# Performance work log

Measured on AMD Instinct MI355X. Metric: run time of the kernel, lower is better.

## Reference

```python
import jax, jax.numpy as jnp
import numpy as np

B, T_AUX, UP = 4, 75, 110
N_AUX, N_Q, HID, SKIP = 54, 256, 192, 256
K, AUX_K = 6, 3
DIL_FACTS = [0, 1, 2] * 3  # dilation_depth=3, dilation_repeat=3
T = T_AUX * UP - 1  # 8249


def conv1d(x, w, b, dil=1, pad=(0, 0)):
    # x: (B,C,T), w: (O,I,K) torch Conv1d layout
    if pad != (0, 0):
        x = jnp.pad(x, ((0, 0), (0, 0), pad))
    y = jax.lax.conv_general_dilated(x, w, (1,), 'VALID', rhs_dilation=(dil,),
                                     dimension_numbers=('NCH', 'OIH', 'NCH'))
    return y + b[None, :, None]


def setup_inputs() -> dict:
    key = jax.random.key(0)
    ks = jax.random.split(key, 24)
    s = 0.05
    inp = {
        'audio': jax.random.normal(ks[0], (B, N_Q, T), jnp.float32),
        'aux': jax.random.normal(ks[1], (B, N_AUX, T_AUX), jnp.float32),
        'scale_in_w': jax.random.normal(ks[2], (N_AUX, N_AUX, 1), jnp.float32) * s,
        'scale_in_b': jax.random.normal(ks[3], (N_AUX,), jnp.float32) * s,
        'aux0_w': jax.random.normal(ks[4], (N_AUX * 3, N_AUX, AUX_K), jnp.float32) * s,
        'aux0_b': jax.random.normal(ks[5], (N_AUX * 3,), jnp.float32) * s,
        'aux1_w': jax.random.normal(ks[6], (N_AUX * 9, N_AUX * 3, AUX_K), jnp.float32) * s,
        'aux1_b': jax.random.normal(ks[7], (N_AUX * 9,), jnp.float32) * s,
        'up_w': jax.random.normal(ks[8], (UP,), jnp.float32) * s,
        'up_b': jax.random.normal(ks[9], (), jnp.float32) * s,
        'causal_w': jax.random.normal(ks[10], (HID, N_Q, K), jnp.float32) * s,
        'causal_b': jax.random.normal(ks[11], (HID,), jnp.float32) * s,
        'inx_w': jax.random.normal(ks[12], (9, 2 * HID, N_AUX * 9, 1), jnp.float32) * s,
        'inx_b': jax.random.normal(ks[13], (9, 2 * HID), jnp.float32) * s,
        'dilh_w': jax.random.normal(ks[14], (9, 2 * HID, HID, K), jnp.float32) * s,
        'dilh_b': jax.random.normal(ks[15], (9, 2 * HID), jnp.float32) * s,
        'skip_w': jax.random.normal(ks[16], (9, SKIP, HID, 1), jnp.float32) * s,
        'skip_b': jax.random.normal(ks[17], (9, SKIP), jnp.float32) * s,
        'out1_w': jax.random.normal(ks[18], (N_Q, SKIP, 1), jnp.float32) * s,
        'out1_b': jax.random.normal(ks[19], (N_Q,), jnp.float32) * s,
        'out2_w': jax.random.normal(ks[20], (N_Q, N_Q, 1), jnp.float32) * s,
        'out2_b': jax.random.normal(ks[21], (N_Q,), jnp.float32) * s,
    }
    return inp


def reference(audio, aux, scale_in_w, scale_in_b, aux0_w, aux0_b, aux1_w, aux1_b,
              up_w, up_b, causal_w, causal_b, inx_w, inx_b, dilh_w, dilh_b,
              skip_w, skip_b, out1_w, out1_b, out2_w, out2_b):
    # conditioning path: scale_in -> two-sided dilated convs -> deconv upsample
    a = conv1d(aux, scale_in_w, scale_in_b)
    a = conv1d(a, aux0_w, aux0_b, dil=1, pad=(1, 1))      # k=3, dil=1, same length
    a = conv1d(a, aux1_w, aux1_b, dil=3, pad=(3, 3))      # k=3, dil=3, same length
    b_, c_, t_ = a.shape
    x = (a[:, :, :, None] * up_w).reshape(b_, c_, t_ * UP) + up_b  # ConvTranspose2d(1,1,(1,UP))
    x = x[:, :, 1:]  # (B, 486, T)
    # audio path: causal conv (left pad k-1) + softsign
    h = jax.nn.soft_sign(conv1d(audio, causal_w, causal_b, dil=1, pad=(K - 1, 0)))
    sum_out = None
    for l, d in enumerate(DIL_FACTS):
        dil = K ** d
        lpad = dil * (K - 1)  # k**(d+1) - k**d
        xh = conv1d(x, inx_w[l], inx_b[l]) * conv1d(h, dilh_w[l], dilh_b[l], dil=dil, pad=(lpad, 0))
        z = jax.nn.sigmoid(xh[:, :HID])
        h = (1.0 - z) * jnp.tanh(xh[:, HID:]) + z * h
        skip = conv1d(h, skip_w[l], skip_b[l])
        sum_out = skip if sum_out is None else sum_out + skip
    out = conv1d(jax.nn.relu(sum_out), out1_w, out1_b)
    out = conv1d(jax.nn.relu(out), out2_w, out2_b)
    return out.transpose(0, 2, 1)  # (B, T, n_quantize)
```

## Files before the change

### kernel.cpp

```cpp
#include <hip/hip_runtime.h>

#define TLEN 8249
#define TPAD 8256
#define NTILES 129
#define NB 4
#define NAUX 54
#define NQ 256
#define HID 192
#define NSKIP 256
#define KW 6
#define UPF 110
#define TAUX 75
#define PADR 180
#define HROWS (PADR + TPAD)

typedef __attribute__((ext_vector_type(8))) short bf16x8v;
typedef __attribute__((ext_vector_type(4))) float f32x4;

__device__ __forceinline__ unsigned short f2bf(float f) {
  unsigned int u = __float_as_uint(f);
  u += 0x7FFFu + ((u >> 16) & 1u);
  return (unsigned short)(u >> 16);
}

__device__ __forceinline__ f32x4 mfma16(bf16x8v a, bf16x8v b, f32x4 c) {
  return __builtin_amdgcn_mfma_f32_16x16x32_bf16(a, b, c, 0, 0, 0);
}

__global__ void prepack_kernel(
    const float* causal_w, const float* dilh_w, const float* skip_w,
    const float* out1_w, const float* out2_w,
    const float* inx_w, const float* inx_b, const float* up_b,
    unsigned short* pk_causal, unsigned short* pk_dilh, unsigned short* pk_skip,
    unsigned short* pk_out1, unsigned short* pk_out2, float* Cbuf)
{
  int i = blockIdx.x * blockDim.x + threadIdx.x;
  if (i < 9*6*6*24*64*8) {
    int t = i;
    int j = t & 7; t >>= 3;
    int lane = t & 63; t >>= 6;
    int nf = t % 24; t /= 24;
    int kc = t % 6; t /= 6;
    int tap = t % 6; t /= 6;
    int l = t;
    int oc = nf*16 + (lane & 15);
    int ic = kc*32 + ((lane >> 4) << 3) + j;
    pk_dilh[i] = f2bf(dilh_w[((l*384 + oc)*HID + ic)*KW + tap]);
  }
  if (i < 6*8*12*64*8) {
    int t = i;
    int j = t & 7; t >>= 3;
    int lane = t & 63; t >>= 6;
    int nf = t % 12; t /= 12;
    int kc = t % 8; t /= 8;
    int tap = t;
    int oc = nf*16 + (lane & 15);
    int ic = kc*32 + ((lane >> 4) << 3) + j;
    pk_causal[i] = f2bf(causal_w[(oc*NQ + ic)*KW + tap]);
  }
  if (i < 9*6*16*64*8) {
    int t = i;
    int j = t & 7; t >>= 3;
    int lane = t & 63; t >>= 6;
    int nf = t % 16; t /= 16;
    int kc = t % 6; t /= 6;
    int l = t;
    int sc = nf*16 + (lane & 15);
    int ic = kc*32 + ((lane >> 4) << 3) + j;
    pk_skip[i] = f2bf(skip_w[(l*NSKIP + sc)*HID + ic]);
  }
  if (i < 8*16*64*8) {
    int t = i;
    int j = t & 7; t >>= 3;
    int lane = t & 63; t >>= 6;
    int nf = t % 16; t /= 16;
    int kc = t;
    int oq = nf*16 + (lane & 15);
    int sc = kc*32 + ((lane >> 4) << 3) + j;
    pk_out1[i] = f2bf(out1_w[oq*NSKIP + sc]);
    pk_out2[i] = f2bf(out2_w[oq*NQ + sc]);
  }
  if (i < 9*384) {
    int l = i / 384, oc = i % 384;
    const float* wr = inx_w + (l*384 + oc)*486;
    float s = 0.f;
    for (int c = 0; c < 486; c++) s += wr[c];
    Cbuf[i] = up_b[0]*s + inx_b[i];
  }
}

__global__ void zpad_kernel(unsigned short* hA, unsigned short* hB) {
  int i = blockIdx.x*blockDim.x + threadIdx.x;
  if (i < NB*PADR*HID) {
    int b = i / (PADR*HID), r = i % (PADR*HID);
    hA[(size_t)(b*HROWS)*HID + r] = 0;
    hB[(size_t)(b*HROWS)*HID + r] = 0;
  }
}

__global__ void aux1_kernel(const float* aux, const float* w, const float* bias, float* a1) {
  int q = blockIdx.x, b = blockIdx.y, co = threadIdx.x;
  if (co >= NAUX) return;
  float acc = bias[co];
  for (int ci = 0; ci < NAUX; ci++)
    acc += w[co*NAUX + ci] * aux[(b*NAUX + ci)*TAUX + q];
  a1[(b*NAUX + co)*TAUX + q] = acc;
}

__global__ void aux2_kernel(const float* a1, const float* w, const float* bias, float* a2) {
  __shared__ float s[3][NAUX];
  int q = blockIdx.x, b = blockIdx.y, tid = threadIdx.x;
  for (int i = tid; i < 3*NAUX; i += blockDim.x) {
    int k = i / NAUX, c = i % NAUX;
    int qq = q - 1 + k;
    s[k][c] = (qq >= 0 && qq < TAUX) ? a1[(b*NAUX + c)*TAUX + qq] : 0.f;
  }
  __syncthreads();
  int co = tid;
  if (co >= 162) return;
  float acc = bias[co];
  for (int c = 0; c < NAUX; c++)
    #pragma unroll
    for (int k = 0; k < 3; k++)
      acc += w[(co*NAUX + c)*3 + k] * s[k][c];
  a2[(b*162 + co)*TAUX + q] = acc;
}

__global__ void aux3_kernel(const float* a2, const float* w, const float* bias, float* a3) {
  __shared__ float s[3][162];
  int q = blockIdx.x, b = blockIdx.y, tid = threadIdx.x;
  for (int i = tid; i < 3*162; i += blockDim.x) {
    int k = i / 162, c = i % 162;
    int qq = q + 3*(k - 1);
    s[k][c] = (qq >= 0 && qq < TAUX) ? a2[(b*162 + c)*TAUX + qq] : 0.f;
  }
  __syncthreads();
  int co = tid;
  if (co >= 486) return;
  float acc = bias[co];
  for (int c = 0; c < 162; c++)
    #pragma unroll
    for (int k = 0; k < 3; k++)
      acc += w[(co*162 + c)*3 + k] * s[k][c];
  a3[(b*486 + co)*TAUX + q] = acc;
}

__global__ void g_kernel(const float* a3, const float* inx_w, float* G) {
  __shared__ float s[486][15];
  int q0 = blockIdx.x * 15, b = blockIdx.y, l = blockIdx.z;
  int tid = threadIdx.x;
  for (int i = tid; i < 486*15; i += 384) {
    int c = i / 15, qq = i % 15;
    s[c][qq] = a3[(b*486 + c)*TAUX + q0 + qq];
  }
  __syncthreads();
  int oc = tid;
  float acc[15];
  #pragma unroll
  for (int qq = 0; qq < 15; qq++) acc[qq] = 0.f;
  const float* wrow = inx_w + (l*384 + oc)*486;
  for (int c = 0; c < 486; c++) {
    float w = wrow[c];
    #pragma unroll
    for (int qq = 0; qq < 15; qq++) acc[qq] += w * s[c][qq];
  }
  for (int qq = 0; qq < 15; qq++)
    G[((size_t)(l*NB + b)*TAUX + q0 + qq)*384 + oc] = acc[qq];
}

__global__ __launch_bounds__(256, 2)
void causal_kernel(const float* audio, const unsigned short* pk, const float* cb,
                   float* hf, unsigned short* hbf)
{
  __shared__ __align__(16) unsigned short sA[72*264];
  int b = blockIdx.y, t0 = blockIdx.x*64, tid = threadIdx.x;
  int wv = tid >> 6, lane = tid & 63, lanelo = lane & 15;

  for (int i = tid; i < 72*256; i += 256) {
    int ic = i / 72, tt = i % 72;
    int t = t0 - 5 + tt;
    float v = (t >= 0 && t < TLEN) ? audio[(size_t)(b*NQ + ic)*TLEN + t] : 0.f;
    sA[tt*264 + ic] = f2bf(v);
  }
  __syncthreads();

  f32x4 acc[4][3];
  f32x4 z4 = {0.f, 0.f, 0.f, 0.f};
  #pragma unroll
  for (int m = 0; m < 4; m++)
    #pragma unroll
    for (int i = 0; i < 3; i++) acc[m][i] = z4;

  for (int tap = 0; tap < 6; tap++) {
    for (int kc = 0; kc < 8; kc++) {
      bf16x8v A[4];
      int ko = kc*32 + ((lane >> 4) << 3);
      #pragma unroll
      for (int m = 0; m < 4; m++)
        A[m] = *(const bf16x8v*)&sA[(m*16 + lanelo + tap)*264 + ko];
      #pragma unroll
      for (int i = 0; i < 3; i++) {
        int nf = wv*3 + i;
        bf16x8v Bf = *(const bf16x8v*)&pk[(size_t)((((tap*8) + kc)*12 + nf)*64 + lane)*8];
        #pragma unroll
        for (int m = 0; m < 4; m++) acc[m][i] = mfma16(A[m], Bf, acc[m][i]);
      }
    }
  }

  #pragma unroll
  for (int m = 0; m < 4; m++)
    #pragma unroll
    for (int i = 0; i < 3; i++) {
      int oc = (wv*3 + i)*16 + lanelo;
      float bias = cb[oc];
      #pragma unroll
      for (int r = 0; r < 4; r++) {
        int tl = m*16 + ((lane >> 4) << 2) + r;
        int t = t0 + tl;
        float v = acc[m][i][r] + bias;
        float h0 = v / (1.f + fabsf(v));
        hf[(size_t)(b*TPAD + t)*HID + oc] = h0;
        hbf[(size_t)(b*HROWS + t + PADR)*HID + oc] = f2bf(h0);
      }
    }
}

__global__ __launch_bounds__(256, 2)
void layer_kernel(int dil, int first,
                  const unsigned short* hin, unsigned short* hout,
                  float* hf, float* sum_out,
                  const unsigned short* pk_dilh_l, const float* dilh_b_l,
                  const unsigned short* pk_skip_l, const float* skip_b_l,
                  const float* Gl, const float* Cl, const float* up_w)
{
  __shared__ __align__(16) unsigned short hs[64*200];
  int b = blockIdx.y, t0 = blockIdx.x*64, tid = threadIdx.x;
  int wv = tid >> 6, lane = tid & 63, lanelo = lane & 15;

  f32x4 accz[4][3], acct[4][3];
  f32x4 z4 = {0.f, 0.f, 0.f, 0.f};
  #pragma unroll
  for (int m = 0; m < 4; m++)
    #pragma unroll
    for (int i = 0; i < 3; i++) { accz[m][i] = z4; acct[m][i] = z4; }

  for (int tap = 0; tap < 6; tap++) {
    __syncthreads();
    int rowbase = t0 + (tap - 5)*dil + PADR;
    for (int i = tid; i < 64*24; i += 256) {
      int r = i / 24, seg = i % 24;
      bf16x8v v = *(const bf16x8v*)&hin[(size_t)(b*HROWS + rowbase + r)*HID + seg*8];
      *(bf16x8v*)&hs[r*200 + seg*8] = v;
    }
    __syncthreads();
    for (int kc = 0; kc < 6; kc++) {
      bf16x8v A[4];
      int ko = kc*32 + ((lane >> 4) << 3);
      #pragma unroll
      for (int m = 0; m < 4; m++)
        A[m] = *(const bf16x8v*)&hs[(m*16 + lanelo)*200 + ko];
      #pragma unroll
      for (int i = 0; i < 3; i++) {
        int nfz = wv*3 + i, nft = 12 + wv*3 + i;
        bf16x8v Bz = *(const bf16x8v*)&pk_dilh_l[(size_t)(((tap*6 + kc)*24 + nfz)*64 + lane)*8];
        bf16x8v Bt = *(const bf16x8v*)&pk_dilh_l[(size_t)(((tap*6 + kc)*24 + nft)*64 + lane)*8];
        #pragma unroll
        for (int m = 0; m < 4; m++) {
          accz[m][i] = mfma16(A[m], Bz, accz[m][i]);
          acct[m][i] = mfma16(A[m], Bt, acct[m][i]);
        }
      }
    }
  }
  __syncthreads();

  #pragma unroll
  for (int m = 0; m < 4; m++) {
    #pragma unroll
    for (int r = 0; r < 4; r++) {
      int tl = m*16 + ((lane >> 4) << 2) + r;
      int t = t0 + tl;
      int tp1 = t + 1;
      int q = tp1 / UPF; if (q > TAUX - 1) q = TAUX - 1;
      int ui = tp1 - q*UPF; if (ui > UPF - 1) ui = UPF - 1;
      float u = up_w[ui];
      const float* Gb = Gl + (size_t)(b*TAUX + q)*384;
      #pragma unroll
      for (int i = 0; i < 3; i++) {
        int ocz = (wv*3 + i)*16 + lanelo;
        float iz = u*Gb[ocz]       + Cl[ocz];
        float it = u*Gb[192 + ocz] + Cl[192 + ocz];
        float xz = (accz[m][i][r] + dilh_b_l[ocz])       * iz;
        float xt = (acct[m][i][r] + dilh_b_l[192 + ocz]) * it;
        float z  = 1.f / (1.f + __expf(-xz));
        float e2 = __expf(2.f*xt);
        float th = 1.f - 2.f/(e2 + 1.f);
        size_t gi = (size_t)(b*TPAD + t)*HID + ocz;
        float hold = hf[gi];
        float hn = (1.f - z)*th + z*hold;
        hf[gi] = hn;
        unsigned short hb = f2bf(hn);
        hout[(size_t)(b*HROWS + t + PADR)*HID + ocz] = hb;
        hs[tl*200 + ocz] = hb;
      }
    }
  }
  __syncthreads();

  f32x4 acc2[4][4];
  #pragma unroll
  for (int m = 0; m < 4; m++)
    #pragma unroll
    for (int i = 0; i < 4; i++) acc2[m][i] = z4;
  for (int kc = 0; kc < 6; kc++) {
    bf16x8v A[4];
    int ko = kc*32 + ((lane >> 4) << 3);
    #pragma unroll
    for (int m = 0; m < 4; m++)
      A[m] = *(const bf16x8v*)&hs[(m*16 + lanelo)*200 + ko];
    #pragma unroll
    for (int i = 0; i < 4; i++) {
      int nf = wv*4 + i;
      bf16x8v Bf = *(const bf16x8v*)&pk_skip_l[(size_t)((kc*16 + nf)*64 + lane)*8];
      #pragma unroll
      for (int m = 0; m < 4; m++) acc2[m][i] = mfma16(A[m], Bf, acc2[m][i]);
    }
  }
  #pragma unroll
  for (int m = 0; m < 4; m++)
    #pragma unroll
    for (int i = 0; i < 4; i++) {
      int sc = (wv*4 + i)*16 + lanelo;
      float bias = skip_b_l[sc];
      #pragma unroll
      for (int r = 0; r < 4; r++) {
        int tl = m*16 + ((lane >> 4) << 2) + r;
        int t = t0 + tl;
        float v = acc2[m][i][r] + bias;
        float* dst = &sum_out[(size_t)(b*TPAD + t)*NSKIP + sc];
        *dst = first ? v : (*dst + v);
      }
    }
}

__global__ __launch_bounds__(256, 2)
void out_kernel(const float* sum_out, const unsigned short* pk1, const float* b1,
                const unsigned short* pk2, const float* b2, float* dout)
{
  __shared__ __align__(16) unsigned short s0[64*264];
  int b = blockIdx.y, t0 = blockIdx.x*64, tid = threadIdx.x;
  int wv = tid >> 6, lane = tid & 63, lanelo = lane & 15;
  f32x4 z4 = {0.f, 0.f, 0.f, 0.f};

  for (int i = tid; i < 64*64; i += 256) {
    int r = i >> 6, cg = i & 63;
    f32x4 v = *(const f32x4*)&sum_out[(size_t)(b*TPAD + t0 + r)*NSKIP + cg*4];
    unsigned int lo = (unsigned int)f2bf(fmaxf(v[0], 0.f)) | ((unsigned int)f2bf(fmaxf(v[1], 0.f)) << 16);
    unsigned int hi = (unsigned int)f2bf(fmaxf(v[2], 0.f)) | ((unsigned int)f2bf(fmaxf(v[3], 0.f)) << 16);
    uint2 pv; pv.x = lo; pv.y = hi;
    *(uint2*)&s0[r*264 + cg*4] = pv;
  }
  __syncthreads();

  f32x4 acc[4][4];
  #pragma unroll
  for (int m = 0; m < 4; m++)
    #pragma unroll
    for (int i = 0; i < 4; i++) acc[m][i] = z4;
  for (int kc = 0; kc < 8; kc++) {
    bf16x8v A[4];
    int ko = kc*32 + ((lane >> 4) << 3);
    #pragma unroll
    for (int m = 0; m < 4; m++)
      A[m] = *(const bf16x8v*)&s0[(m*16 + lanelo)*264 + ko];
    #pragma unroll
    for (int i = 0; i < 4; i++) {
      int nf = wv*4 + i;
      bf16x8v Bf = *(const bf16x8v*)&pk1[(size_t)((kc*16 + nf)*64 + lane)*8];
      #pragma unroll
      for (int m = 0; m < 4; m++) acc[m][i] = mfma16(A[m], Bf, acc[m][i]);
    }
  }
  __syncthreads();
  #pragma unroll
  for (int m = 0; m < 4; m++)
    #pragma unroll
    for (int i = 0; i < 4; i++) {
      int oq = (wv*4 + i)*16 + lanelo;
      float bias = b1[oq];
      #pragma unroll
      for (int r = 0; r < 4; r++) {
        int tl = m*16 + ((lane >> 4) << 2) + r;
        float v = acc[m][i][r] + bias;
        s0[tl*264 + oq] = f2bf(fmaxf(v, 0.f));
      }
    }
  __syncthreads();

  #pragma unroll
  for (int m = 0; m < 4; m++)
    #pragma unroll
    for (int i = 0; i < 4; i++) acc[m][i] = z4;
  for (int kc = 0; kc < 8; kc++) {
    bf16x8v A[4];
    int ko = kc*32 + ((lane >> 4) << 3);
    #pragma unroll
    for (int m = 0; m < 4; m++)
      A[m] = *(const bf16x8v*)&s0[(m*16 + lanelo)*264 + ko];
    #pragma unroll
    for (int i = 0; i < 4; i++) {
      int nf = wv*4 + i;
      bf16x8v Bf = *(const bf16x8v*)&pk2[(size_t)((kc*16 + nf)*64 + lane)*8];
      #pragma unroll
      for (int m = 0; m < 4; m++) acc[m][i] = mfma16(A[m], Bf, acc[m][i]);
    }
  }
  #pragma unroll
  for (int m = 0; m < 4; m++)
    #pragma unroll
    for (int i = 0; i < 4; i++) {
      int oq = (wv*4 + i)*16 + lanelo;
      float bias = b2[oq];
      #pragma unroll
      for (int r = 0; r < 4; r++) {
        int tl = m*16 + ((lane >> 4) << 2) + r;
        int t = t0 + tl;
        if (t < TLEN) dout[(size_t)(b*TLEN + t)*NQ + oq] = acc[m][i][r] + bias;
      }
    }
}

extern "C" void kernel_launch(void* const* d_in, const int* in_sizes, int n_in,
                              void* d_out, int out_size, void* d_ws, size_t ws_size,
                              hipStream_t stream)
{
  const float* audio      = (const float*)d_in[0];
  const float* aux        = (const float*)d_in[1];
  const float* scale_in_w = (const float*)d_in[2];
  const float* scale_in_b = (const float*)d_in[3];
  const float* aux0_w     = (const float*)d_in[4];
  const float* aux0_b     = (const float*)d_in[5];
  const float* aux1_w     = (const float*)d_in[6];
  const float* aux1_b     = (const float*)d_in[7];
  const float* up_w       = (const float*)d_in[8];
  const float* up_b       = (const float*)d_in[9];
  const float* causal_w   = (const float*)d_in[10];
  const float* causal_b   = (const float*)d_in[11];
  const float* inx_w      = (const float*)d_in[12];
  const float* inx_b      = (const float*)d_in[13];
  const float* dilh_w     = (const float*)d_in[14];
  const float* dilh_b     = (const float*)d_in[15];
  const float* skip_w     = (const float*)d_in[16];
  const float* skip_b     = (const float*)d_in[17];
  const float* out1_w     = (const float*)d_in[18];
  const float* out1_b     = (const float*)d_in[19];
  const float* out2_w     = (const float*)d_in[20];
  const float* out2_b     = (const float*)d_in[21];

  char* ws = (char*)d_ws;
  size_t off = 0;
  auto alloc = [&](size_t bytes) -> void* {
    void* p = ws + off;
    off += (bytes + 255) & ~(size_t)255;
    return p;
  };
  unsigned short* pk_causal = (unsigned short*)alloc((size_t)6*8*12*64*8*2);
  unsigned short* pk_dilh   = (unsigned short*)alloc((size_t)9*6*6*24*64*8*2);
  unsigned short* pk_skip   = (unsigned short*)alloc((size_t)9*6*16*64*8*2);
  unsigned short* pk_out1   = (unsigned short*)alloc((size_t)8*16*64*8*2);
  unsigned short* pk_out2   = (unsigned short*)alloc((size_t)8*16*64*8*2);
  float* Cbuf    = (float*)alloc((size_t)9*384*4);
  float* a1      = (float*)alloc((size_t)NB*NAUX*TAUX*4);
  float* a2      = (float*)alloc((size_t)NB*162*TAUX*4);
  float* a3      = (float*)alloc((size_t)NB*486*TAUX*4);
  float* Gbuf    = (float*)alloc((size_t)9*NB*TAUX*384*4);
  unsigned short* hbfA = (unsigned short*)alloc((size_t)NB*HROWS*HID*2);
  unsigned short* hbfB = (unsigned short*)alloc((size_t)NB*HROWS*HID*2);
  float* hf      = (float*)alloc((size_t)NB*TPAD*HID*4);
  float* sum_out = (float*)alloc((size_t)NB*TPAD*NSKIP*4);

  hipLaunchKernelGGL(prepack_kernel, dim3((9*6*6*24*64*8 + 255)/256), dim3(256), 0, stream,
                     causal_w, dilh_w, skip_w, out1_w, out2_w, inx_w, inx_b, up_b,
                     pk_causal, pk_dilh, pk_skip, pk_out1, pk_out2, Cbuf);
  hipLaunchKernelGGL(zpad_kernel, dim3((NB*PADR*HID + 255)/256), dim3(256), 0, stream,
                     hbfA, hbfB);
  hipLaunchKernelGGL(aux1_kernel, dim3(TAUX, NB), dim3(64), 0, stream,
                     aux, scale_in_w, scale_in_b, a1);
  hipLaunchKernelGGL(aux2_kernel, dim3(TAUX, NB), dim3(192), 0, stream,
                     a1, aux0_w, aux0_b, a2);
  hipLaunchKernelGGL(aux3_kernel, dim3(TAUX, NB), dim3(512), 0, stream,
                     a2, aux1_w, aux1_b, a3);
  hipLaunchKernelGGL(g_kernel, dim3(5, NB, 9), dim3(384), 0, stream,
                     a3, inx_w, Gbuf);
  hipLaunchKernelGGL(causal_kernel, dim3(NTILES, NB), dim3(256), 0, stream,
                     audio, pk_causal, causal_b, hf, hbfA);

  const int dils[9] = {1, 6, 36, 1, 6, 36, 1, 6, 36};
  for (int l = 0; l < 9; l++) {
    const unsigned short* hin = (l & 1) ? hbfB : hbfA;
    unsigned short* hout      = (l & 1) ? hbfA : hbfB;
    hipLaunchKernelGGL(layer_kernel, dim3(NTILES, NB), dim3(256), 0, stream,
                       dils[l], (l == 0) ? 1 : 0,
                       hin, hout, hf, sum_out,
                       pk_dilh + (size_t)l*6*6*24*64*8,
                       dilh_b + (size_t)l*384,
                       pk_skip + (size_t)l*6*16*64*8,
                       skip_b + (size_t)l*256,
                       Gbuf + (size_t)l*NB*TAUX*384,
                       Cbuf + (size_t)l*384,
                       up_w);
  }

  hipLaunchKernelGGL(out_kernel, dim3(NTILES, NB), dim3(256), 0, stream,
                     sum_out, pk_out1, out1_b, pk_out2, out2_b, (float*)d_out);
}
```

Before: 1.046 ms.

## Stage full dilated halo once per larger tile and drop fp32 hidden state

After: 1.191 ms. +13.9%, slower.

```diff
diff --git a/kernel.cpp b/kernel.cpp
--- a/kernel.cpp
+++ b/kernel.cpp
@@ -1,8 +1,10 @@
 #include <hip/hip_runtime.h>
 
 #define TLEN 8249
-#define TPAD 8256
-#define NTILES 129
+#define TPAD 8320
+#define NTILES_L 52
+#define NTILES_64 130
+#define MTILE 160
 #define NB 4
 #define NAUX 54
 #define NQ 256
@@ -170,7 +172,7 @@
 
 __global__ __launch_bounds__(256, 2)
 void causal_kernel(const float* audio, const unsigned short* pk, const float* cb,
-                   float* hf, unsigned short* hbf)
+                   unsigned short* hbf)
 {
   __shared__ __align__(16) unsigned short sA[72*264];
   int b = blockIdx.y, t0 = blockIdx.x*64, tid = threadIdx.x;
@@ -220,66 +222,73 @@
         int t = t0 + tl;
         float v = acc[m][i][r] + bias;
         float h0 = v / (1.f + fabsf(v));
-        hf[(size_t)(b*TPAD + t)*HID + oc] = h0;
         hbf[(size_t)(b*HROWS + t + PADR)*HID + oc] = f2bf(h0);
       }
     }
 }
 
-__global__ __launch_bounds__(256, 2)
+__global__ __launch_bounds__(512, 1)
 void layer_kernel(int dil, int first,
                   const unsigned short* hin, unsigned short* hout,
-                  float* hf, float* sum_out,
+                  float* sum_out,
                   const unsigned short* pk_dilh_l, const float* dilh_b_l,
                   const unsigned short* pk_skip_l, const float* skip_b_l,
                   const float* Gl, const float* Cl, const float* up_w)
 {
-  __shared__ __align__(16) unsigned short hs[64*200];
-  int b = blockIdx.y, t0 = blockIdx.x*64, tid = threadIdx.x;
-  int wv = tid >> 6, lane = tid & 63, lanelo = lane & 15;
-
-  f32x4 accz[4][3], acct[4][3];
+  extern __shared__ __align__(16) unsigned short hs[];
+  int b = blockIdx.y, t0 = blockIdx.x*MTILE, tid = threadIdx.x;
+  int wv = tid >> 6, lane = tid & 63, lanelo = lane & 15, lanehi = lane >> 4;
+  int mwv = wv >> 2, nwv = wv & 3;
+
+  int W = MTILE + 5*dil;
+  int rowbase = t0 - 5*dil + PADR;
+  for (int i = tid; i < W*24; i += 512) {
+    int r = i / 24, seg = i % 24;
+    bf16x8v v = *(const bf16x8v*)&hin[(size_t)(b*HROWS + rowbase + r)*HID + seg*8];
+    *(bf16x8v*)&hs[r*200 + seg*8] = v;
+  }
+  __syncthreads();
+
+  f32x4 accz[5][3], acct[5][3];
   f32x4 z4 = {0.f, 0.f, 0.f, 0.f};
   #pragma unroll
-  for (int m = 0; m < 4; m++)
+  for (int m = 0; m < 5; m++)
     #pragma unroll
     for (int i = 0; i < 3; i++) { accz[m][i] = z4; acct[m][i] = z4; }
 
+  int tl0 = mwv*80 + lanelo;
   for (int tap = 0; tap < 6; tap++) {
-    __syncthreads();
-    int rowbase = t0 + (tap - 5)*dil + PADR;
-    for (int i = tid; i < 64*24; i += 256) {
-      int r = i / 24, seg = i % 24;
-      bf16x8v v = *(const bf16x8v*)&hin[(size_t)(b*HROWS + rowbase + r)*HID + seg*8];
-      *(bf16x8v*)&hs[r*200 + seg*8] = v;
-    }
-    __syncthreads();
+    int rb = (tl0 + tap*dil)*200;
+    #pragma unroll
     for (int kc = 0; kc < 6; kc++) {
-      bf16x8v A[4];
-      int ko = kc*32 + ((lane >> 4) << 3);
-      #pragma unroll
-      for (int m = 0; m < 4; m++)
-        A[m] = *(const bf16x8v*)&hs[(m*16 + lanelo)*200 + ko];
+      bf16x8v A[5];
+      int ko = kc*32 + (lanehi << 3);
+      #pragma unroll
+      for (int m = 0; m < 5; m++)
+        A[m] = *(const bf16x8v*)&hs[rb + m*3200 + ko];
       #pragma unroll
       for (int i = 0; i < 3; i++) {
-        int nfz = wv*3 + i, nft = 12 + wv*3 + i;
-        bf16x8v Bz = *(const bf16x8v*)&pk_dilh_l[(size_t)(((tap*6 + kc)*24 + nfz)*64 + lane)*8];
-        bf16x8v Bt = *(const bf16x8v*)&pk_dilh_l[(size_t)(((tap*6 + kc)*24 + nft)*64 + lane)*8];
+        const unsigned short* bp =
+            &pk_dilh_l[(size_t)(((tap*6 + kc)*24 + nwv*3 + i)*64 + lane)*8];
+        bf16x8v Bz = *(const bf16x8v*)bp;
+        bf16x8v Bt = *(const bf16x8v*)(bp + 12*512);
         #pragma unroll
-        for (int m = 0; m < 4; m++) {
+        for (int m = 0; m < 5; m++) {
           accz[m][i] = mfma16(A[m], Bz, accz[m][i]);
           acct[m][i] = mfma16(A[m], Bt, acct[m][i]);
         }
       }
     }
   }
-  __syncthreads();
-
-  #pragma unroll
-  for (int m = 0; m < 4; m++) {
+
+  int hnb = (dil == 36) ? 0 : W;
+  if (dil == 36) __syncthreads();
+
+  #pragma unroll
+  for (int m = 0; m < 5; m++) {
     #pragma unroll
     for (int r = 0; r < 4; r++) {
-      int tl = m*16 + ((lane >> 4) << 2) + r;
+      int tl = mwv*80 + m*16 + (lanehi << 2) + r;
       int t = t0 + tl;
       int tp1 = t + 1;
       int q = tp1 / UPF; if (q > TAUX - 1) q = TAUX - 1;
@@ -288,7 +297,7 @@
       const float* Gb = Gl + (size_t)(b*TAUX + q)*384;
       #pragma unroll
       for (int i = 0; i < 3; i++) {
-        int ocz = (wv*3 + i)*16 + lanelo;
+        int ocz = (nwv*3 + i)*16 + lanelo;
         float iz = u*Gb[ocz]       + Cl[ocz];
         float it = u*Gb[192 + ocz] + Cl[192 + ocz];
         float xz = (accz[m][i][r] + dilh_b_l[ocz])       * iz;
@@ -296,49 +305,48 @@
         float z  = 1.f / (1.f + __expf(-xz));
         float e2 = __expf(2.f*xt);
         float th = 1.f - 2.f/(e2 + 1.f);
-        size_t gi = (size_t)(b*TPAD + t)*HID + ocz;
-        float hold = hf[gi];
+        unsigned short hob = hs[(tl + 5*dil)*200 + ocz];
+        float hold = __uint_as_float(((unsigned int)hob) << 16);
         float hn = (1.f - z)*th + z*hold;
-        hf[gi] = hn;
         unsigned short hb = f2bf(hn);
         hout[(size_t)(b*HROWS + t + PADR)*HID + ocz] = hb;
-        hs[tl*200 + ocz] = hb;
-      }
-    }
-  }
-  __syncthreads();
-
-  f32x4 acc2[4][4];
-  #pragma unroll
-  for (int m = 0; m < 4; m++)
+        hs[(hnb + tl)*200 + ocz] = hb;
+      }
+    }
+  }
+  __syncthreads();
+
+  f32x4 acc2[5][4];
+  #pragma unroll
+  for (int m = 0; m < 5; m++)
     #pragma unroll
     for (int i = 0; i < 4; i++) acc2[m][i] = z4;
+  int rbs = (hnb + mwv*80 + lanelo)*200;
+  #pragma unroll
   for (int kc = 0; kc < 6; kc++) {
-    bf16x8v A[4];
-    int ko = kc*32 + ((lane >> 4) << 3);
-    #pragma unroll
-    for (int m = 0; m < 4; m++)
-      A[m] = *(const bf16x8v*)&hs[(m*16 + lanelo)*200 + ko];
+    bf16x8v A[5];
+    int ko = kc*32 + (lanehi << 3);
+    #pragma unroll
+    for (int m = 0; m < 5; m++)
+      A[m] = *(const bf16x8v*)&hs[rbs + m*3200 + ko];
     #pragma unroll
     for (int i = 0; i < 4; i++) {
-      int nf = wv*4 + i;
-      bf16x8v Bf = *(const bf16x8v*)&pk_skip_l[(size_t)((kc*16 + nf)*64 + lane)*8];
-      #pragma unroll
-      for (int m = 0; m < 4; m++) acc2[m][i] = mfma16(A[m], Bf, acc2[m][i]);
-    }
-  }
-  #pragma unroll
-  for (int m = 0; m < 4; m++)
+      bf16x8v Bf = *(const bf16x8v*)&pk_skip_l[(size_t)((kc*16 + nwv*4 + i)*64 + lane)*8];
+      #pragma unroll
+      for (int m = 0; m < 5; m++) acc2[m][i] = mfma16(A[m], Bf, acc2[m][i]);
+    }
+  }
+  #pragma unroll
+  for (int m = 0; m < 5; m++)
     #pragma unroll
     for (int i = 0; i < 4; i++) {
-      int sc = (wv*4 + i)*16 + lanelo;
+      int sc = (nwv*4 + i)*16 + lanelo;
       float bias = skip_b_l[sc];
       #pragma unroll
       for (int r = 0; r < 4; r++) {
-        int tl = m*16 + ((lane >> 4) << 2) + r;
-        int t = t0 + tl;
+        int tl = mwv*80 + m*16 + (lanehi << 2) + r;
         float v = acc2[m][i][r] + bias;
-        float* dst = &sum_out[(size_t)(b*TPAD + t)*NSKIP + sc];
+        float* dst = &sum_out[(size_t)(b*TPAD + t0 + tl)*NSKIP + sc];
         *dst = first ? v : (*dst + v);
       }
     }
@@ -477,8 +485,10 @@
   float* Gbuf    = (float*)alloc((size_t)9*NB*TAUX*384*4);
   unsigned short* hbfA = (unsigned short*)alloc((size_t)NB*HROWS*HID*2);
   unsigned short* hbfB = (unsigned short*)alloc((size_t)NB*HROWS*HID*2);
-  float* hf      = (float*)alloc((size_t)NB*TPAD*HID*4);
   float* sum_out = (float*)alloc((size_t)NB*TPAD*NSKIP*4);
+
+  hipFuncSetAttribute((const void*)layer_kernel,
+                      hipFuncAttributeMaxDynamicSharedMemorySize, 140000);
 
   hipLaunchKernelGGL(prepack_kernel, dim3((9*6*6*24*64*8 + 255)/256), dim3(256), 0, stream,
                      causal_w, dilh_w, skip_w, out1_w, out2_w, inx_w, inx_b, up_b,
@@ -493,16 +503,18 @@
                      a2, aux1_w, aux1_b, a3);
   hipLaunchKernelGGL(g_kernel, dim3(5, NB, 9), dim3(384), 0, stream,
                      a3, inx_w, Gbuf);
-  hipLaunchKernelGGL(causal_kernel, dim3(NTILES, NB), dim3(256), 0, stream,
-                     audio, pk_causal, causal_b, hf, hbfA);
+  hipLaunchKernelGGL(causal_kernel, dim3(NTILES_64, NB), dim3(256), 0, stream,
+                     audio, pk_causal, causal_b, hbfA);
 
   const int dils[9] = {1, 6, 36, 1, 6, 36, 1, 6, 36};
   for (int l = 0; l < 9; l++) {
     const unsigned short* hin = (l & 1) ? hbfB : hbfA;
     unsigned short* hout      = (l & 1) ? hbfA : hbfB;
-    hipLaunchKernelGGL(layer_kernel, dim3(NTILES, NB), dim3(256), 0, stream,
+    int W = MTILE + 5*dils[l];
+    int ldsb = (W + ((dils[l] == 36) ? 0 : MTILE)) * 200 * 2;
+    hipLaunchKernelGGL(layer_kernel, dim3(NTILES_L, NB), dim3(512), ldsb, stream,
                        dils[l], (l == 0) ? 1 : 0,
-                       hin, hout, hf, sum_out,
+                       hin, hout, sum_out,
                        pk_dilh + (size_t)l*6*6*24*64*8,
                        dilh_b + (size_t)l*384,
                        pk_skip + (size_t)l*6*16*64*8,
@@ -512,6 +524,6 @@
                        up_w);
   }
 
-  hipLaunchKernelGGL(out_kernel, dim3(NTILES, NB), dim3(256), 0, stream,
+  hipLaunchKernelGGL(out_kernel, dim3(NTILES_64, NB), dim3(256), 0, stream,
                      sum_out, pk_out1, out1_b, pk_out2, out2_b, (float*)d_out);
 }
```
